# Optimization experiments

Measured on AMD Instinct MI355X. Metric: run time of the kernel, lower is better.

The kernel has to match this reference:

```python
import jax, jax.numpy as jnp
import numpy as np

N = 131072      # total nodes
G = 1024        # graphs
NPG = 128       # nodes per graph (equal-sized graphs, batch sorted)
E = 2097152     # edges (avg degree 16)
H = 64          # hidden_channels
K = 30          # sort-pool k
MAXZ = 1000     # max_z
D = 3 * H + 1   # total_latent_dim = hidden*num_layers + 1 = 193
DENSE = ((K - 2) // 2 + 1 - 5 + 1) * 32  # 352


def setup_inputs():
    key = jax.random.key(0)
    ks = jax.random.split(key, 16)
    z = jax.random.randint(ks[0], (N,), 0, MAXZ)
    # within-graph random edges
    g = jax.random.randint(ks[1], (E,), 0, G)
    src = g * NPG + jax.random.randint(ks[2], (E,), 0, NPG)
    dst = g * NPG + jax.random.randint(ks[3], (E,), 0, NPG)
    edge_index = jnp.stack([src, dst])
    batch = jnp.repeat(jnp.arange(G), NPG)

    def w(k, shape, fan):
        return jax.random.normal(k, shape, dtype=jnp.float32) / np.float32(np.sqrt(fan))

    z_table = w(ks[4], (MAXZ, H), H)
    W0 = w(ks[5], (H, H), H); b0 = jnp.zeros((H,), jnp.float32)
    W1 = w(ks[6], (H, H), H); b1 = jnp.zeros((H,), jnp.float32)
    W2 = w(ks[7], (H, H), H); b2 = jnp.zeros((H,), jnp.float32)
    W3 = w(ks[8], (H, 1), H); b3 = jnp.zeros((1,), jnp.float32)
    conv1_w = w(ks[9], (16, D), D); conv1_b = jnp.zeros((16,), jnp.float32)
    conv2_w = w(ks[10], (32, 16, 5), 16 * 5); conv2_b = jnp.zeros((32,), jnp.float32)
    lin1_w = w(ks[11], (DENSE, 128), DENSE); lin1_b = jnp.zeros((128,), jnp.float32)
    lin2_w = w(ks[12], (128, 1), 128); lin2_b = jnp.zeros((1,), jnp.float32)
    return dict(z=z, edge_index=edge_index, batch=batch, z_table=z_table,
                W0=W0, b0=b0, W1=W1, b1=b1, W2=W2, b2=b2, W3=W3, b3=b3,
                conv1_w=conv1_w, conv1_b=conv1_b, conv2_w=conv2_w, conv2_b=conv2_b,
                lin1_w=lin1_w, lin1_b=lin1_b, lin2_w=lin2_w, lin2_b=lin2_b)


def _forward(z, edge_index, z_table, W0, b0, W1, b1, W2, b2, W3, b3,
             conv1_w, conv1_b, conv2_w, conv2_b, lin1_w, lin1_b, lin2_w, lin2_b):
    src, dst = edge_index[0], edge_index[1]
    loop = jnp.arange(N)
    src_sl = jnp.concatenate([src, loop])  # self-loops (gcn_norm)
    dst_sl = jnp.concatenate([dst, loop])
    deg = jax.ops.segment_sum(jnp.ones((E + N,), jnp.float32), dst_sl, num_segments=N)
    dinv = jnp.where(deg > 0, 1.0 / jnp.sqrt(deg), 0.0)
    norm = dinv[src_sl] * dinv[dst_sl]  # sym-normalized edge weights

    def gcn(x, W, b):
        h = x @ W
        agg = jax.ops.segment_sum(h[src_sl] * norm[:, None], dst_sl, num_segments=N)
        return agg + b

    x = z_table[z]  # z_embedding lookup, [N, H]
    xs = []
    for W, b in ((W0, b0), (W1, b1), (W2, b2), (W3, b3)):
        x = jnp.tanh(gcn(x, W, b))
        xs.append(x)
    xc = jnp.concatenate(xs, axis=-1)  # [N, D] (concat of xs[1:])

    # global_sort_pool: sort per graph by last channel (descending), keep top-K.
    xg = xc.reshape(G, NPG, D)
    order = jnp.argsort(-xg[:, :, -1], axis=1)[:, :K]
    topk = jnp.take_along_axis(xg, order[:, :, None], axis=1)  # [G, K, D]

    # conv1: kernel=stride=D over flattened [G, 1, K*D] == per-node linear D->16
    h1 = jax.nn.relu(jnp.einsum('gkd,cd->gck', topk, conv1_w) + conv1_b[None, :, None])  # [G,16,K]
    p = h1.reshape(G, 16, K // 2, 2).max(-1)  # maxpool1d(2,2) -> [G,16,15]
    h2 = jax.nn.relu(
        jax.lax.conv_general_dilated(p, conv2_w, (1,), 'VALID',
                                     dimension_numbers=('NCH', 'OIH', 'NCH'))
        + conv2_b[None, :, None])  # [G,32,11]
    flat = h2.reshape(G, -1)  # channel-major flatten, matches torch .view
    hm = jax.nn.relu(flat @ lin1_w + lin1_b)  # MLP (dropout off in eval)
    return hm @ lin2_w + lin2_b  # [G, 1]


def reference(z, edge_index, batch, z_table, W0, b0, W1, b1, W2, b2, W3, b3,
              conv1_w, conv1_b, conv2_w, conv2_b, lin1_w, lin1_b, lin2_w, lin2_b):
    del batch  # graphs are equal-sized & node ids contiguous: reshape implements sort-pool segmentation
    return _forward(z, edge_index, z_table, W0, b0, W1, b1, W2, b2, W3, b3,
                    conv1_w, conv1_b, conv2_w, conv2_b, lin1_w, lin1_b, lin2_w, lin2_b)
```

## Files before the change

### kernel.cpp

```cpp
#include <hip/hip_runtime.h>

#define NGRAPH  1024
#define E_EDGES 2097152
#define ECAP    2944
#define MAXZ    1000

__device__ __forceinline__ float bfu_lo(unsigned u) { return __uint_as_float(u << 16); }
__device__ __forceinline__ float bfu_hi(unsigned u) { return __uint_as_float(u & 0xFFFF0000u); }
__device__ __forceinline__ unsigned packlo(float f0, float f1) {
    return (__float_as_uint(f0) >> 16) | (__float_as_uint(f1) & 0xFFFF0000u);
}
__device__ __forceinline__ int xh_idx(int r, int k)  { return (r << 6) | (k  ^ ((r & 7) << 3)); }
__device__ __forceinline__ int xl_idx(int r, int k2) { return (r << 5) | (k2 ^ ((r & 7) << 2)); }

__device__ __forceinline__ double tanh_fast(double p) {
    double q = 2.0 * p;
    q = fmin(40.0, fmax(-40.0, q));
    double nf = rint(q * 1.4426950408889634074);
    double r  = fma(nf, -6.93147180369123816490e-01, q);
    r = fma(nf, -1.90821492927058770002e-10, r);
    double er =     2.755731922398589e-07;
    er = fma(er, r, 2.755731922398589e-06);
    er = fma(er, r, 2.4801587301587302e-05);
    er = fma(er, r, 1.984126984126984e-04);
    er = fma(er, r, 1.3888888888888889e-03);
    er = fma(er, r, 8.333333333333333e-03);
    er = fma(er, r, 4.1666666666666664e-02);
    er = fma(er, r, 1.6666666666666666e-01);
    er = fma(er, r, 0.5);
    er = fma(er, r, 1.0);
    er = fma(er, r, 1.0);
    double E = er * __longlong_as_double((long long)(1023 + (int)nf) << 52);
    return 1.0 - 2.0 / (E + 1.0);
}

__global__ void markWS_kernel(float* out) {
    int i = blockIdx.x * 256 + threadIdx.x;
    if (i < NGRAPH) out[i] = 2.0f;
}

__global__ void adjscatter_kernel(const int* __restrict__ ei,
                                  unsigned* __restrict__ adjG) {
    int e = blockIdx.x * 256 + threadIdx.x;
    if (e >= E_EDGES) return;
    int s = ei[e];
    int d = ei[E_EDGES + e];
    int g = s >> 7;
    int sl = s & 127, dl = d & 127;
    atomicAdd(&adjG[((size_t)g << 12) + (dl << 5) + (sl >> 2)], 1u << ((sl & 3) << 3));
}

__global__ __launch_bounds__(1024, 1) void gnn2_kernel(
    const int* __restrict__ z,
    const unsigned* __restrict__ adjG,
    const float* __restrict__ zt,
    const float* __restrict__ W0, const float* __restrict__ b0,
    const float* __restrict__ W1, const float* __restrict__ b1,
    const float* __restrict__ W2, const float* __restrict__ b2,
    const float* __restrict__ W3, const float* __restrict__ b3,
    const float* __restrict__ c1w, const float* __restrict__ c1b,
    const float* __restrict__ c2w, const float* __restrict__ c2b,
    const float* __restrict__ l1w, const float* __restrict__ l1b,
    const float* __restrict__ l2w, const float* __restrict__ l2b,
    float* __restrict__ xdump,
    float* __restrict__ out)
{
    __shared__ __align__(16) float    Xhi[2][8192];
    __shared__ __align__(16) unsigned Xlo[2][4096];
    __shared__ unsigned char  csr[2][ECAP];
    __shared__ unsigned short rp16[2][132];
    __shared__ int            aux[2][128];
    __shared__ int            inv[2][30];
    __shared__ float          kd30f[2][30];
    __shared__ int            w0tot[2];

    const int half = threadIdx.x >> 9;
    const int tt   = threadIdx.x & 511;
    const int g    = (blockIdx.x << 1) | half;
    const int r0 = tt >> 3;
    const int r1 = r0 + 64;
    const int c0 = (tt & 7) << 3;

    float*          XH = Xhi[half];
    unsigned*       XL = Xlo[half];
    unsigned char*  CS = csr[half];
    unsigned short* RP = rp16[half];
    int*            AX = aux[half];

    unsigned* adjM = (unsigned*)XH;

    {
        const uint4* src = (const uint4*)(adjG + ((size_t)g << 12));
        uint4* dst = (uint4*)adjM;
        for (int i = tt; i < 1024; i += 512) dst[i] = src[i];
    }
    if (tt < 30) { inv[half][tt] = tt; kd30f[half][tt] = 0.f; }
    __syncthreads();

    int degv = 0;
    if (tt < 128) {
        for (int w = 0; w < 32; ++w) {
            unsigned u = adjM[(tt << 5) + w];
            degv += (int)((u & 255u) + ((u >> 8) & 255u) + ((u >> 16) & 255u) + (u >> 24));
        }
        AX[tt] = degv;
    }
    if (tt < 128) {
        int v = degv;
        for (int o = 1; o < 64; o <<= 1) {
            int u = __shfl_up(v, o, 64);
            if ((tt & 63) >= o) v += u;
        }
        if (tt == 63) w0tot[half] = v;
        RP[tt + 1] = (unsigned short)v;
    }
    __syncthreads();
    if (tt >= 64 && tt < 128) RP[tt + 1] = (unsigned short)(RP[tt + 1] + w0tot[half]);
    if (tt == 0) RP[0] = 0;
    __syncthreads();

    const int mydeg = (tt < 128) ? AX[tt] : 0;
    const double dv0 = 1.0 / sqrt((double)(AX[r0] + 1));
    const double dv1 = 1.0 / sqrt((double)(AX[r1] + 1));
    const double dvm = 1.0 / sqrt((double)(mydeg + 1));

    if (tt < 128) {
        unsigned pos = RP[tt];
        for (int w = 0; w < 32; ++w) {
            unsigned u = adjM[(tt << 5) + w];
            while (u) {
                int b2 = (u & 0xFFu) ? 0 : (u & 0xFF00u) ? 1 : (u & 0xFF0000u) ? 2 : 3;
                int m = (int)((u >> (b2 << 3)) & 255u);
                unsigned char sv = (unsigned char)((w << 2) + b2);
                for (int q = 0; q < m; ++q) { if (pos < ECAP) CS[pos] = sv; ++pos; }
                u &= ~(0xFFu << (b2 << 3));
            }
        }
    }
    __syncthreads();

    for (int idx = tt; idx < 8192; idx += 512) {
        int n = idx >> 6, c = idx & 63;
        int zv = z[(g << 7) + n];
        zv = (zv < 0) ? 0 : ((zv >= MAXZ) ? MAXZ - 1 : zv);
        XH[xh_idx(n, c)] = zt[zv * 64 + c];
    }
    __syncthreads();

    for (int layer = 0; layer < 3; ++layer) {
        const float* Wg = (layer == 0) ? W0 : (layer == 1) ? W1 : W2;
        const float* bg = (layer == 0) ? b0 : (layer == 1) ? b1 : b2;
        const bool haslo = (layer != 0);

        double accd0[8], accd1[8]; float accf0[8], accf1[8];
#pragma unroll
        for (int j = 0; j < 8; ++j) { accd0[j] = 0.0; accd1[j] = 0.0; accf0[j] = 0.f; accf1[j] = 0.f; }

        for (int k = 0; k < 64; k += 4) {
            float4 a0 = *(const float4*)&XH[xh_idx(r0, k)];
            float4 a1 = *(const float4*)&XH[xh_idx(r1, k)];
            float x0[4] = {a0.x, a0.y, a0.z, a0.w};
            float x1[4] = {a1.x, a1.y, a1.z, a1.w};
            float l0[4], l1[4];
            if (haslo) {
                uint2 u0 = *(const uint2*)&XL[xl_idx(r0, k >> 1)];
                uint2 u1 = *(const uint2*)&XL[xl_idx(r1, k >> 1)];
                l0[0] = bfu_lo(u0.x); l0[1] = bfu_hi(u0.x); l0[2] = bfu_lo(u0.y); l0[3] = bfu_hi(u0.y);
                l1[0] = bfu_lo(u1.x); l1[1] = bfu_hi(u1.x); l1[2] = bfu_lo(u1.y); l1[3] = bfu_hi(u1.y);
            }
#pragma unroll
            for (int kk = 0; kk < 4; ++kk) {
                const float* wr = Wg + ((k + kk) << 6) + c0;
                float4 wa = *(const float4*)wr;
                float4 wb = *(const float4*)(wr + 4);
                float wf[8] = {wa.x, wa.y, wa.z, wa.w, wb.x, wb.y, wb.z, wb.w};
                double xd0 = (double)x0[kk], xd1 = (double)x1[kk];
#pragma unroll
                for (int j = 0; j < 8; ++j) {
                    double wd = (double)wf[j];
                    accd0[j] = fma(xd0, wd, accd0[j]);
                    accd1[j] = fma(xd1, wd, accd1[j]);
                }
                if (haslo) {
#pragma unroll
                    for (int j = 0; j < 8; ++j) {
                        accf0[j] = fmaf(l0[kk], wf[j], accf0[j]);
                        accf1[j] = fmaf(l1[kk], wf[j], accf1[j]);
                    }
                }
            }
        }
        __syncthreads();

        float hfv[2][8], rsv[2][8];
#pragma unroll
        for (int rw = 0; rw < 2; ++rw) {
            int rr = rw ? r1 : r0;
            double dv = rw ? dv1 : dv0;
#pragma unroll
            for (int j = 0; j < 8; ++j) {
                double acc = rw ? (accd1[j] + (double)accf1[j]) : (accd0[j] + (double)accf0[j]);
                double h = dv * acc;
                float hf = (float)h;
                hfv[rw][j] = hf;
                rsv[rw][j] = (float)(h - (double)hf);
            }
            int bi = xh_idx(rr, c0);
            *(float4*)&XH[bi]     = make_float4(hfv[rw][0], hfv[rw][1], hfv[rw][2], hfv[rw][3]);
            *(float4*)&XH[bi + 4] = make_float4(hfv[rw][4], hfv[rw][5], hfv[rw][6], hfv[rw][7]);
            uint4 lv;
            lv.x = packlo(rsv[rw][0], rsv[rw][1]);
            lv.y = packlo(rsv[rw][2], rsv[rw][3]);
            lv.z = packlo(rsv[rw][4], rsv[rw][5]);
            lv.w = packlo(rsv[rw][6], rsv[rw][7]);
            *(uint4*)&XL[xl_idx(rr, c0 >> 1)] = lv;
        }
        __syncthreads();

        double ad[2][8]; float af[2][8];
#pragma unroll
        for (int rw = 0; rw < 2; ++rw)
#pragma unroll
            for (int j = 0; j < 8; ++j) { ad[rw][j] = (double)hfv[rw][j]; af[rw][j] = rsv[rw][j]; }

#pragma unroll
        for (int rw = 0; rw < 2; ++rw) {
            int rr = rw ? r1 : r0;
            for (unsigned e = RP[rr]; e < RP[rr + 1]; ++e) {
                int s = CS[e];
                int bi = (s << 6) | (c0 ^ ((s & 7) << 3));
                float4 a = *(const float4*)&XH[bi];
                float4 b = *(const float4*)&XH[bi + 4];
                uint4 lu = *(const uint4*)&XL[(s << 5) | ((c0 >> 1) ^ ((s & 7) << 2))];
                ad[rw][0] += (double)a.x; ad[rw][1] += (double)a.y;
                ad[rw][2] += (double)a.z; ad[rw][3] += (double)a.w;
                ad[rw][4] += (double)b.x; ad[rw][5] += (double)b.y;
                ad[rw][6] += (double)b.z; ad[rw][7] += (double)b.w;
                af[rw][0] += bfu_lo(lu.x); af[rw][1] += bfu_hi(lu.x);
                af[rw][2] += bfu_lo(lu.y); af[rw][3] += bfu_hi(lu.y);
                af[rw][4] += bfu_lo(lu.z); af[rw][5] += bfu_hi(lu.z);
                af[rw][6] += bfu_lo(lu.w); af[rw][7] += bfu_hi(lu.w);
            }
        }
        __syncthreads();

#pragma unroll
        for (int rw = 0; rw < 2; ++rw) {
            int rr = rw ? r1 : r0;
            double dv = rw ? dv1 : dv0;
            float vf[8], rs[8];
#pragma unroll
            for (int j = 0; j < 8; ++j) {
                double v = tanh_fast(dv * (ad[rw][j] + (double)af[rw][j]) + (double)bg[c0 + j]);
                float vfl = (float)v;
                vf[j] = vfl;
                rs[j] = (float)(v - (double)vfl);
            }
            int bi = xh_idx(rr, c0);
            *(float4*)&XH[bi]     = make_float4(vf[0], vf[1], vf[2], vf[3]);
            *(float4*)&XH[bi + 4] = make_float4(vf[4], vf[5], vf[6], vf[7]);
            uint4 lv;
            lv.x = packlo(rs[0], rs[1]);
            lv.y = packlo(rs[2], rs[3]);
            lv.z = packlo(rs[4], rs[5]);
            lv.w = packlo(rs[6], rs[7]);
            *(uint4*)&XL[xl_idx(rr, c0 >> 1)] = lv;

            if (layer < 2) {
                float* xd = xdump + (((size_t)g * 2 + layer) << 13) + (rr << 6) + c0;
                *(float4*)xd       = make_float4(vf[0], vf[1], vf[2], vf[3]);
                *(float4*)(xd + 4) = make_float4(vf[4], vf[5], vf[6], vf[7]);
            }
        }
        __syncthreads();
    }

    double* h4sD  = (double*)XL;
    double* keydD = ((double*)XL) + 128;

    double sdreg = 0.0;
    if (tt < 128) {
        double sd = 0.0; float sf = 0.f;
        for (int k = 0; k < 64; k += 4) {
            float4 a = *(const float4*)&XH[xh_idx(tt, k)];
            uint2  u = *(const uint2*)&XL[xl_idx(tt, k >> 1)];
            float4 w = *(const float4*)&W3[k];
            sd = fma((double)a.x, (double)w.x, sd);
            sd = fma((double)a.y, (double)w.y, sd);
            sd = fma((double)a.z, (double)w.z, sd);
            sd = fma((double)a.w, (double)w.w, sd);
            sf = fmaf(bfu_lo(u.x), w.x, sf);
            sf = fmaf(bfu_hi(u.x), w.y, sf);
            sf = fmaf(bfu_lo(u.y), w.z, sf);
            sf = fmaf(bfu_hi(u.y), w.w, sf);
        }
        sdreg = sd + (double)sf;
    }
    __syncthreads();
    if (tt < 128) h4sD[tt] = dvm * sdreg;
    __syncthreads();
    double keyreg = 0.0;
    if (tt < 128) {
        double a = h4sD[tt];
        for (unsigned e = RP[tt]; e < RP[tt + 1]; ++e) a += h4sD[CS[e]];
        keyreg = tanh_fast(dvm * a + (double)b3[0]);
        keydD[tt] = keyreg;
    }
    __syncthreads();

    if (tt < 128) {
        int rk = 0;
        for (int j = 0; j < 128; ++j) {
            double kj = keydD[j];
            if (kj > keyreg || (kj == keyreg && j < tt)) ++rk;
        }
        if (rk < 30) { inv[half][rk] = tt; kd30f[half][rk] = (float)keyreg; }
    }
    __syncthreads();

    float* XloF = (float*)XL;
    float* h1v = XloF + 2560;
    float* ppv = XloF + 3040;
    float* flv = XloF + 3280;
    float* hmv = XloF + 3632;

    if (tt < 480) {
        int c = tt & 15, k = tt >> 4;
        int node = inv[half][k];
        const float* wrow = c1w + c * 193;
        const float* xg0 = xdump + ((size_t)g * 2) * 8192 + node * 64;
        const float* xg1 = xg0 + 8192;
        float s8[8];
#pragma unroll
        for (int cg = 0; cg < 8; ++cg) {
            float acc = 0.f;
            float4 xa = *(const float4*)&xg0[cg * 8];
            float4 xb = *(const float4*)&xg0[cg * 8 + 4];
            const float* w0p = wrow + cg * 8;
            acc = fmaf(xa.x, w0p[0], acc); acc = fmaf(xa.y, w0p[1], acc);
            acc = fmaf(xa.z, w0p[2], acc); acc = fmaf(xa.w, w0p[3], acc);
            acc = fmaf(xb.x, w0p[4], acc); acc = fmaf(xb.y, w0p[5], acc);
            acc = fmaf(xb.z, w0p[6], acc); acc = fmaf(xb.w, w0p[7], acc);
            float4 ya = *(const float4*)&xg1[cg * 8];
            float4 yb = *(const float4*)&xg1[cg * 8 + 4];
            const float* w1p = wrow + 64 + cg * 8;
            acc = fmaf(ya.x, w1p[0], acc); acc = fmaf(ya.y, w1p[1], acc);
            acc = fmaf(ya.z, w1p[2], acc); acc = fmaf(ya.w, w1p[3], acc);
            acc = fmaf(yb.x, w1p[4], acc); acc = fmaf(yb.y, w1p[5], acc);
            acc = fmaf(yb.z, w1p[6], acc); acc = fmaf(yb.w, w1p[7], acc);
            const float* w2p = wrow + 128 + cg * 8;
#pragma unroll
            for (int j = 0; j < 8; ++j)
                acc = fmaf(XH[xh_idx(node, cg * 8 + j)], w2p[j], acc);
            s8[cg] = acc;
        }
        float A0 = s8[0] + s8[1], A1 = s8[2] + s8[3];
        float A2 = s8[4] + s8[5], A3 = s8[6] + s8[7];
        float G = (A0 + A1) + (A2 + A3);
        float s = G + c1w[c * 193 + 192] * kd30f[half][k] + c1b[c];
        h1v[c * 30 + k] = s > 0.f ? s : 0.f;
    }
    __syncthreads();
    if (tt < 240) {
        int c = tt & 15, i = tt >> 4;
        float a = h1v[c * 30 + 2 * i], b = h1v[c * 30 + 2 * i + 1];
        ppv[c * 15 + i] = a > b ? a : b;
    }
    __syncthreads();
    if (tt < 352) {
        int o = tt / 11, j = tt % 11;
        float s = c2b[o];
        for (int i = 0; i < 16; ++i)
#pragma unroll
            for (int u = 0; u < 5; ++u)
                s = fmaf(ppv[i * 15 + j + u], c2w[o * 80 + i * 5 + u], s);
        flv[tt] = s > 0.f ? s : 0.f;
    }
    __syncthreads();
    if (tt < 128) {
        float s = l1b[tt];
        for (int i = 0; i < 352; ++i) s = fmaf(flv[i], l1w[i * 128 + tt], s);
        hmv[tt] = s > 0.f ? s : 0.f;
    }
    __syncthreads();
    if (tt < 64) {
        float v = fmaf(hmv[tt], l2w[tt], hmv[tt + 64] * l2w[tt + 64]);
#pragma unroll
        for (int o = 32; o > 0; o >>= 1) v += __shfl_down(v, o, 64);
        if (tt == 0) out[g] = v + l2b[0];
    }
}

__global__ __launch_bounds__(512, 2) void gnn_kernel(
    const int* __restrict__ z,
    const unsigned* __restrict__ adjG,
    const float* __restrict__ zt,
    const float* __restrict__ W0, const float* __restrict__ b0,
    const float* __restrict__ W1, const float* __restrict__ b1,
    const float* __restrict__ W2, const float* __restrict__ b2,
    const float* __restrict__ W3, const float* __restrict__ b3,
    const float* __restrict__ c1w, const float* __restrict__ c1b,
    const float* __restrict__ c2w, const float* __restrict__ c2b,
    const float* __restrict__ l1w, const float* __restrict__ l1b,
    const float* __restrict__ l2w, const float* __restrict__ l2b,
    float* __restrict__ out)
{
    __shared__ __align__(16) float    Xhi[8192];
    __shared__ __align__(16) unsigned Xlo[4096];
    __shared__ unsigned char  csr[ECAP];
    __shared__ unsigned short rp16[132];
    __shared__ int            aux[128];
    __shared__ int            inv[30];
    __shared__ float          kd30f[30];
    __shared__ int            w0tot;

    const int g  = blockIdx.x;
    const int t  = threadIdx.x;
    const int r0 = t >> 3;
    const int r1 = r0 + 64;
    const int c0 = (t & 7) << 3;

    unsigned* adjM = (unsigned*)Xhi;

    {
        const uint4* src = (const uint4*)(adjG + ((size_t)g << 12));
        uint4* dst = (uint4*)adjM;
        for (int i = t; i < 1024; i += 512) dst[i] = src[i];
    }
    if (t < 30) { inv[t] = t; kd30f[t] = 0.f; }
    __syncthreads();

    int degv = 0;
    if (t < 128) {
        for (int w = 0; w < 32; ++w) {
            unsigned u = adjM[(t << 5) + w];
            degv += (int)((u & 255u) + ((u >> 8) & 255u) + ((u >> 16) & 255u) + (u >> 24));
        }
        aux[t] = degv;
    }
    if (t < 128) {
        int v = degv;
        for (int o = 1; o < 64; o <<= 1) {
            int u = __shfl_up(v, o, 64);
            if ((t & 63) >= o) v += u;
        }
        if (t == 63) w0tot = v;
        rp16[t + 1] = (unsigned short)v;
    }
    __syncthreads();
    if (t >= 64 && t < 128) rp16[t + 1] = (unsigned short)(rp16[t + 1] + w0tot);
    if (t == 0) rp16[0] = 0;
    __syncthreads();

    const int mydeg = (t < 128) ? aux[t] : 0;
    const double dv0 = 1.0 / sqrt((double)(aux[r0] + 1));
    const double dv1 = 1.0 / sqrt((double)(aux[r1] + 1));
    const double dvm = 1.0 / sqrt((double)(mydeg + 1));

    if (t < 128) {
        unsigned pos = rp16[t];
        for (int w = 0; w < 32; ++w) {
            unsigned u = adjM[(t << 5) + w];
            while (u) {
                int b2 = (u & 0xFFu) ? 0 : (u & 0xFF00u) ? 1 : (u & 0xFF0000u) ? 2 : 3;
                int m = (int)((u >> (b2 << 3)) & 255u);
                unsigned char sv = (unsigned char)((w << 2) + b2);
                for (int q = 0; q < m; ++q) { if (pos < ECAP) csr[pos] = sv; ++pos; }
                u &= ~(0xFFu << (b2 << 3));
            }
        }
    }
    __syncthreads();

    for (int idx = t; idx < 8192; idx += 512) {
        int n = idx >> 6, c = idx & 63;
        int zv = z[(g << 7) + n];
        zv = (zv < 0) ? 0 : ((zv >= MAXZ) ? MAXZ - 1 : zv);
        Xhi[xh_idx(n, c)] = zt[zv * 64 + c];
    }
    __syncthreads();

    float g1p[2][16];
#pragma unroll
    for (int rw = 0; rw < 2; ++rw)
#pragma unroll
        for (int c = 0; c < 16; ++c) g1p[rw][c] = 0.f;

    for (int layer = 0; layer < 3; ++layer) {
        const float* Wg = (layer == 0) ? W0 : (layer == 1) ? W1 : W2;
        const float* bg = (layer == 0) ? b0 : (layer == 1) ? b1 : b2;
        const bool haslo = (layer != 0);

        double accd0[8], accd1[8]; float accf0[8], accf1[8];
#pragma unroll
        for (int j = 0; j < 8; ++j) { accd0[j] = 0.0; accd1[j] = 0.0; accf0[j] = 0.f; accf1[j] = 0.f; }

        for (int k = 0; k < 64; k += 4) {
            float4 a0 = *(const float4*)&Xhi[xh_idx(r0, k)];
            float4 a1 = *(const float4*)&Xhi[xh_idx(r1, k)];
            float x0[4] = {a0.x, a0.y, a0.z, a0.w};
            float x1[4] = {a1.x, a1.y, a1.z, a1.w};
            float l0[4], l1[4];
            if (haslo) {
                uint2 u0 = *(const uint2*)&Xlo[xl_idx(r0, k >> 1)];
                uint2 u1 = *(const uint2*)&Xlo[xl_idx(r1, k >> 1)];
                l0[0] = bfu_lo(u0.x); l0[1] = bfu_hi(u0.x); l0[2] = bfu_lo(u0.y); l0[3] = bfu_hi(u0.y);
                l1[0] = bfu_lo(u1.x); l1[1] = bfu_hi(u1.x); l1[2] = bfu_lo(u1.y); l1[3] = bfu_hi(u1.y);
            }
#pragma unroll
            for (int kk = 0; kk < 4; ++kk) {
                const float* wr = Wg + ((k + kk) << 6) + c0;
                float4 wa = *(const float4*)wr;
                float4 wb = *(const float4*)(wr + 4);
                float wf[8] = {wa.x, wa.y, wa.z, wa.w, wb.x, wb.y, wb.z, wb.w};
                double xd0 = (double)x0[kk], xd1 = (double)x1[kk];
#pragma unroll
                for (int j = 0; j < 8; ++j) {
                    double wd = (double)wf[j];
                    accd0[j] = fma(xd0, wd, accd0[j]);
                    accd1[j] = fma(xd1, wd, accd1[j]);
                }
                if (haslo) {
#pragma unroll
                    for (int j = 0; j < 8; ++j) {
                        accf0[j] = fmaf(l0[kk], wf[j], accf0[j]);
                        accf1[j] = fmaf(l1[kk], wf[j], accf1[j]);
                    }
                }
            }
        }
        __syncthreads();

        float hfv[2][8], rsv[2][8];
#pragma unroll
        for (int rw = 0; rw < 2; ++rw) {
            int rr = rw ? r1 : r0;
            double dv = rw ? dv1 : dv0;
#pragma unroll
            for (int j = 0; j < 8; ++j) {
                double acc = rw ? (accd1[j] + (double)accf1[j]) : (accd0[j] + (double)accf0[j]);
                double h = dv * acc;
                float hf = (float)h;
                hfv[rw][j] = hf;
                rsv[rw][j] = (float)(h - (double)hf);
            }
            int bi = xh_idx(rr, c0);
            *(float4*)&Xhi[bi]     = make_float4(hfv[rw][0], hfv[rw][1], hfv[rw][2], hfv[rw][3]);
            *(float4*)&Xhi[bi + 4] = make_float4(hfv[rw][4], hfv[rw][5], hfv[rw][6], hfv[rw][7]);
            uint4 lv;
            lv.x = packlo(rsv[rw][0], rsv[rw][1]);
            lv.y = packlo(rsv[rw][2], rsv[rw][3]);
            lv.z = packlo(rsv[rw][4], rsv[rw][5]);
            lv.w = packlo(rsv[rw][6], rsv[rw][7]);
            *(uint4*)&Xlo[xl_idx(rr, c0 >> 1)] = lv;
        }
        __syncthreads();

        double ad[2][8]; float af[2][8];
#pragma unroll
        for (int rw = 0; rw < 2; ++rw)
#pragma unroll
            for (int j = 0; j < 8; ++j) { ad[rw][j] = (double)hfv[rw][j]; af[rw][j] = rsv[rw][j]; }

#pragma unroll
        for (int rw = 0; rw < 2; ++rw) {
            int rr = rw ? r1 : r0;
            for (unsigned e = rp16[rr]; e < rp16[rr + 1]; ++e) {
                int s = csr[e];
                int bi = (s << 6) | (c0 ^ ((s & 7) << 3));
                float4 a = *(const float4*)&Xhi[bi];
                float4 b = *(const float4*)&Xhi[bi + 4];
                uint4 lu = *(const uint4*)&Xlo[(s << 5) | ((c0 >> 1) ^ ((s & 7) << 2))];
                ad[rw][0] += (double)a.x; ad[rw][1] += (double)a.y;
                ad[rw][2] += (double)a.z; ad[rw][3] += (double)a.w;
                ad[rw][4] += (double)b.x; ad[rw][5] += (double)b.y;
                ad[rw][6] += (double)b.z; ad[rw][7] += (double)b.w;
                af[rw][0] += bfu_lo(lu.x); af[rw][1] += bfu_hi(lu.x);
                af[rw][2] += bfu_lo(lu.y); af[rw][3] += bfu_hi(lu.y);
                af[rw][4] += bfu_lo(lu.z); af[rw][5] += bfu_hi(lu.z);
                af[rw][6] += bfu_lo(lu.w); af[rw][7] += bfu_hi(lu.w);
            }
        }
        __syncthreads();

#pragma unroll
        for (int rw = 0; rw < 2; ++rw) {
            int rr = rw ? r1 : r0;
            double dv = rw ? dv1 : dv0;
            float vf[8], rs[8];
#pragma unroll
            for (int j = 0; j < 8; ++j) {
                double v = tanh_fast(dv * (ad[rw][j] + (double)af[rw][j]) + (double)bg[c0 + j]);
                float vfl = (float)v;
                vf[j] = vfl;
                rs[j] = (float)(v - (double)vfl);
            }
            int bi = xh_idx(rr, c0);
            *(float4*)&Xhi[bi]     = make_float4(vf[0], vf[1], vf[2], vf[3]);
            *(float4*)&Xhi[bi + 4] = make_float4(vf[4], vf[5], vf[6], vf[7]);
            uint4 lv;
            lv.x = packlo(rs[0], rs[1]);
            lv.y = packlo(rs[2], rs[3]);
            lv.z = packlo(rs[4], rs[5]);
            lv.w = packlo(rs[6], rs[7]);
            *(uint4*)&Xlo[xl_idx(rr, c0 >> 1)] = lv;

            const float* w1base = c1w + layer * 64 + c0;
            for (int c = 0; c < 16; ++c) {
                const float* wr = w1base + c * 193;
#pragma unroll
                for (int j = 0; j < 8; ++j)
                    g1p[rw][c] = fmaf(vf[j], wr[j], g1p[rw][c]);
            }
        }
        __syncthreads();
    }

    double* h4sD  = (double*)Xlo;
    double* keydD = ((double*)Xlo) + 128;

    double sdreg = 0.0;
    if (t < 128) {
        double sd = 0.0; float sf = 0.f;
        for (int k = 0; k < 64; k += 4) {
            float4 a = *(const float4*)&Xhi[xh_idx(t, k)];
            uint2  u = *(const uint2*)&Xlo[xl_idx(t, k >> 1)];
            float4 w = *(const float4*)&W3[k];
            sd = fma((double)a.x, (double)w.x, sd);
            sd = fma((double)a.y, (double)w.y, sd);
            sd = fma((double)a.z, (double)w.z, sd);
            sd = fma((double)a.w, (double)w.w, sd);
            sf = fmaf(bfu_lo(u.x), w.x, sf);
            sf = fmaf(bfu_hi(u.x), w.y, sf);
            sf = fmaf(bfu_lo(u.y), w.z, sf);
            sf = fmaf(bfu_hi(u.y), w.w, sf);
        }
        sdreg = sd + (double)sf;
    }
    __syncthreads();
    if (t < 128) h4sD[t] = dvm * sdreg;
    __syncthreads();
    double keyreg = 0.0;
    if (t < 128) {
        double a = h4sD[t];
        for (unsigned e = rp16[t]; e < rp16[t + 1]; ++e) a += h4sD[csr[e]];
        keyreg = tanh_fast(dvm * a + (double)b3[0]);
        keydD[t] = keyreg;
    }
    __syncthreads();

    if (t < 128) {
        int rk = 0;
        for (int j = 0; j < 128; ++j) {
            double kj = keydD[j];
            if (kj > keyreg || (kj == keyreg && j < t)) ++rk;
        }
        if (rk < 30) { inv[rk] = t; kd30f[rk] = (float)keyreg; }
    }

#pragma unroll
    for (int m = 1; m <= 4; m <<= 1) {
#pragma unroll
        for (int rw = 0; rw < 2; ++rw)
#pragma unroll
            for (int c = 0; c < 16; ++c)
                g1p[rw][c] += __shfl_xor(g1p[rw][c], m, 64);
    }
    __syncthreads();
    float* XloF = (float*)Xlo;
    float* G1   = XloF + 512;
    if ((t & 7) == 0) {
#pragma unroll
        for (int c = 0; c < 16; c += 4) {
            *(float4*)&G1[r0 * 16 + c] = make_float4(g1p[0][c], g1p[0][c + 1], g1p[0][c + 2], g1p[0][c + 3]);
            *(float4*)&G1[r1 * 16 + c] = make_float4(g1p[1][c], g1p[1][c + 1], g1p[1][c + 2], g1p[1][c + 3]);
        }
    }
    __syncthreads();

    float* h1v = XloF + 2560;
    float* ppv = XloF + 3040;
    float* flv = XloF + 3280;
    float* hmv = XloF + 3632;

    if (t < 480) {
        int c = t & 15, k = t >> 4;
        int node = inv[k];
        float s = G1[node * 16 + c] + c1w[c * 193 + 192] * kd30f[k] + c1b[c];
        h1v[c * 30 + k] = s > 0.f ? s : 0.f;
    }
    __syncthreads();
    if (t < 240) {
        int c = t & 15, i = t >> 4;
        float a = h1v[c * 30 + 2 * i], b = h1v[c * 30 + 2 * i + 1];
        ppv[c * 15 + i] = a > b ? a : b;
    }
    __syncthreads();
    if (t < 352) {
        int o = t / 11, j = t % 11;
        float s = c2b[o];
        for (int i = 0; i < 16; ++i)
#pragma unroll
            for (int u = 0; u < 5; ++u)
                s = fmaf(ppv[i * 15 + j + u], c2w[o * 80 + i * 5 + u], s);
        flv[t] = s > 0.f ? s : 0.f;
    }
    __syncthreads();
    if (t < 128) {
        float s = l1b[t];
        for (int i = 0; i < 352; ++i) s = fmaf(flv[i], l1w[i * 128 + t], s);
        hmv[t] = s > 0.f ? s : 0.f;
    }
    __syncthreads();
    if (t < 64) {
        float v = fmaf(hmv[t], l2w[t], hmv[t + 64] * l2w[t + 64]);
#pragma unroll
        for (int o = 32; o > 0; o >>= 1) v += __shfl_down(v, o, 64);
        if (t == 0) out[g] = v + l2b[0];
    }
}


extern "C" void kernel_launch(void* const* d_in, const int* in_sizes, int n_in,
                              void* d_out, int out_size, void* d_ws, size_t ws_size,
                              hipStream_t stream) {
    const int*   z   = (const int*)d_in[0];
    const int*   ei  = (const int*)d_in[1];
    const float* zt  = (const float*)d_in[3];
    const float* W0  = (const float*)d_in[4];
    const float* b0  = (const float*)d_in[5];
    const float* W1  = (const float*)d_in[6];
    const float* b1  = (const float*)d_in[7];
    const float* W2  = (const float*)d_in[8];
    const float* b2  = (const float*)d_in[9];
    const float* W3  = (const float*)d_in[10];
    const float* b3  = (const float*)d_in[11];
    const float* c1w = (const float*)d_in[12];
    const float* c1b = (const float*)d_in[13];
    const float* c2w = (const float*)d_in[14];
    const float* c2b = (const float*)d_in[15];
    const float* l1w = (const float*)d_in[16];
    const float* l1b = (const float*)d_in[17];
    const float* l2w = (const float*)d_in[18];
    const float* l2b = (const float*)d_in[19];
    float* out = (float*)d_out;

    const size_t ADJ_B = (size_t)NGRAPH * 4096 * 4;
    const size_t XD_B  = (size_t)NGRAPH * 2 * 8192 * 4;
    if (ws_size < ADJ_B) {
        markWS_kernel<<<4, 256, 0, stream>>>(out);
        return;
    }

    unsigned* adjG = (unsigned*)d_ws;

    hipMemsetAsync(adjG, 0, ADJ_B, stream);
    adjscatter_kernel<<<(E_EDGES + 255) / 256, 256, 0, stream>>>(ei, adjG);

    if (ws_size >= ADJ_B + XD_B) {
        float* xdump = (float*)((char*)d_ws + ADJ_B);
        gnn2_kernel<<<NGRAPH / 2, 1024, 0, stream>>>(z, adjG, zt,
                                                     W0, b0, W1, b1, W2, b2, W3, b3,
                                                     c1w, c1b, c2w, c2b, l1w, l1b, l2w, l2b,
                                                     xdump, out);
    } else {
        gnn_kernel<<<NGRAPH, 512, 0, stream>>>(z, adjG, zt,
                                               W0, b0, W1, b1, W2, b2, W3, b3,
                                               c1w, c1b, c2w, c2b, l1w, l1b, l2w, l2b,
                                               out);
    }
}
```

Baseline: 599.7 us.

## Process one graph per 1024-thread block with one node row per thread

The main kernel previously packed two graphs into each 1024-thread block, so each thread handled two node rows. It now launches one block per graph with 1024 threads, and each thread owns a single row. This halves the per-thread register state (double accumulators) and the serial edge-gather length, and it doubles the grid size. The cost is that shared memory per block is halved, so occupancy depends on whether two blocks can co-reside under launch_bounds(1024,1), and the serial tail phases now leave more threads idle per graph.

```diff
diff --git a/kernel.cpp b/kernel.cpp
--- a/kernel.cpp
+++ b/kernel.cpp
@@ -50,7 +50,7 @@
     atomicAdd(&adjG[((size_t)g << 12) + (dl << 5) + (sl >> 2)], 1u << ((sl & 3) << 3));
 }
 
-__global__ __launch_bounds__(1024, 1) void gnn2_kernel(
+__global__ __launch_bounds__(1024, 1) void gnn1k_kernel(
     const int* __restrict__ z,
     const unsigned* __restrict__ adjG,
     const float* __restrict__ zt,
@@ -65,85 +65,75 @@
     float* __restrict__ xdump,
     float* __restrict__ out)
 {
-    __shared__ __align__(16) float    Xhi[2][8192];
-    __shared__ __align__(16) unsigned Xlo[2][4096];
-    __shared__ unsigned char  csr[2][ECAP];
-    __shared__ unsigned short rp16[2][132];
-    __shared__ int            aux[2][128];
-    __shared__ int            inv[2][30];
-    __shared__ float          kd30f[2][30];
-    __shared__ int            w0tot[2];
-
-    const int half = threadIdx.x >> 9;
-    const int tt   = threadIdx.x & 511;
-    const int g    = (blockIdx.x << 1) | half;
-    const int r0 = tt >> 3;
-    const int r1 = r0 + 64;
-    const int c0 = (tt & 7) << 3;
-
-    float*          XH = Xhi[half];
-    unsigned*       XL = Xlo[half];
-    unsigned char*  CS = csr[half];
-    unsigned short* RP = rp16[half];
-    int*            AX = aux[half];
-
-    unsigned* adjM = (unsigned*)XH;
+    __shared__ __align__(16) float    Xhi[8192];
+    __shared__ __align__(16) unsigned Xlo[4096];
+    __shared__ unsigned char  csr[ECAP];
+    __shared__ unsigned short rp16[132];
+    __shared__ int            aux[128];
+    __shared__ int            inv[30];
+    __shared__ float          kd30f[30];
+    __shared__ int            w0tot;
+
+    const int g  = blockIdx.x;
+    const int t  = threadIdx.x;
+    const int r  = t >> 3;
+    const int c0 = (t & 7) << 3;
+
+    unsigned* adjM = (unsigned*)Xhi;
 
     {
         const uint4* src = (const uint4*)(adjG + ((size_t)g << 12));
-        uint4* dst = (uint4*)adjM;
-        for (int i = tt; i < 1024; i += 512) dst[i] = src[i];
-    }
-    if (tt < 30) { inv[half][tt] = tt; kd30f[half][tt] = 0.f; }
+        ((uint4*)adjM)[t & 1023] = src[t & 1023];
+    }
+    if (t < 30) { inv[t] = t; kd30f[t] = 0.f; }
     __syncthreads();
 
     int degv = 0;
-    if (tt < 128) {
+    if (t < 128) {
         for (int w = 0; w < 32; ++w) {
-            unsigned u = adjM[(tt << 5) + w];
+            unsigned u = adjM[(t << 5) + w];
             degv += (int)((u & 255u) + ((u >> 8) & 255u) + ((u >> 16) & 255u) + (u >> 24));
         }
-        AX[tt] = degv;
-    }
-    if (tt < 128) {
+        aux[t] = degv;
+    }
+    if (t < 128) {
         int v = degv;
         for (int o = 1; o < 64; o <<= 1) {
             int u = __shfl_up(v, o, 64);
-            if ((tt & 63) >= o) v += u;
-        }
-        if (tt == 63) w0tot[half] = v;
-        RP[tt + 1] = (unsigned short)v;
-    }
-    __syncthreads();
-    if (tt >= 64 && tt < 128) RP[tt + 1] = (unsigned short)(RP[tt + 1] + w0tot[half]);
-    if (tt == 0) RP[0] = 0;
-    __syncthreads();
-
-    const int mydeg = (tt < 128) ? AX[tt] : 0;
-    const double dv0 = 1.0 / sqrt((double)(AX[r0] + 1));
-    const double dv1 = 1.0 / sqrt((double)(AX[r1] + 1));
+            if ((t & 63) >= o) v += u;
+        }
+        if (t == 63) w0tot = v;
+        rp16[t + 1] = (unsigned short)v;
+    }
+    __syncthreads();
+    if (t >= 64 && t < 128) rp16[t + 1] = (unsigned short)(rp16[t + 1] + w0tot);
+    if (t == 0) rp16[0] = 0;
+    __syncthreads();
+
+    const int mydeg = (t < 128) ? aux[t] : 0;
+    const double dvr = 1.0 / sqrt((double)(aux[r] + 1));
     const double dvm = 1.0 / sqrt((double)(mydeg + 1));
 
-    if (tt < 128) {
-        unsigned pos = RP[tt];
+    if (t < 128) {
+        unsigned pos = rp16[t];
         for (int w = 0; w < 32; ++w) {
-            unsigned u = adjM[(tt << 5) + w];
+            unsigned u = adjM[(t << 5) + w];
             while (u) {
                 int b2 = (u & 0xFFu) ? 0 : (u & 0xFF00u) ? 1 : (u & 0xFF0000u) ? 2 : 3;
                 int m = (int)((u >> (b2 << 3)) & 255u);
                 unsigned char sv = (unsigned char)((w << 2) + b2);
-                for (int q = 0; q < m; ++q) { if (pos < ECAP) CS[pos] = sv; ++pos; }
+                for (int q = 0; q < m; ++q) { if (pos < ECAP) csr[pos] = sv; ++pos; }
                 u &= ~(0xFFu << (b2 << 3));
             }
         }
     }
     __syncthreads();
 
-    for (int idx = tt; idx < 8192; idx += 512) {
+    for (int idx = t; idx < 8192; idx += 1024) {
         int n = idx >> 6, c = idx & 63;
         int zv = z[(g << 7) + n];
         zv = (zv < 0) ? 0 : ((zv >= MAXZ) ? MAXZ - 1 : zv);
-        XH[xh_idx(n, c)] = zt[zv * 64 + c];
+        Xhi[xh_idx(n, c)] = zt[zv * 64 + c];
     }
     __syncthreads();
 
@@ -152,21 +142,17 @@
         const float* bg = (layer == 0) ? b0 : (layer == 1) ? b1 : b2;
         const bool haslo = (layer != 0);
 
-        double accd0[8], accd1[8]; float accf0[8], accf1[8];
-#pragma unroll
-        for (int j = 0; j < 8; ++j) { accd0[j] = 0.0; accd1[j] = 0.0; accf0[j] = 0.f; accf1[j] = 0.f; }
+        double accd[8]; float accf[8];
+#pragma unroll
+        for (int j = 0; j < 8; ++j) { accd[j] = 0.0; accf[j] = 0.f; }
 
         for (int k = 0; k < 64; k += 4) {
-            float4 a0 = *(const float4*)&XH[xh_idx(r0, k)];
-            float4 a1 = *(const float4*)&XH[xh_idx(r1, k)];
+            float4 a0 = *(const float4*)&Xhi[xh_idx(r, k)];
             float x0[4] = {a0.x, a0.y, a0.z, a0.w};
-            float x1[4] = {a1.x, a1.y, a1.z, a1.w};
-            float l0[4], l1[4];
+            float l0[4];
             if (haslo) {
-                uint2 u0 = *(const uint2*)&XL[xl_idx(r0, k >> 1)];
-                uint2 u1 = *(const uint2*)&XL[xl_idx(r1, k >> 1)];
+                uint2 u0 = *(const uint2*)&Xlo[xl_idx(r, k >> 1)];
                 l0[0] = bfu_lo(u0.x); l0[1] = bfu_hi(u0.x); l0[2] = bfu_lo(u0.y); l0[3] = bfu_hi(u0.y);
-                l1[0] = bfu_lo(u1.x); l1[1] = bfu_hi(u1.x); l1[2] = bfu_lo(u1.y); l1[3] = bfu_hi(u1.y);
             }
 #pragma unroll
             for (int kk = 0; kk < 4; ++kk) {
@@ -174,100 +160,82 @@
                 float4 wa = *(const float4*)wr;
                 float4 wb = *(const float4*)(wr + 4);
                 float wf[8] = {wa.x, wa.y, wa.z, wa.w, wb.x, wb.y, wb.z, wb.w};
-                double xd0 = (double)x0[kk], xd1 = (double)x1[kk];
-#pragma unroll
-                for (int j = 0; j < 8; ++j) {
-                    double wd = (double)wf[j];
-                    accd0[j] = fma(xd0, wd, accd0[j]);
-                    accd1[j] = fma(xd1, wd, accd1[j]);
+                double xd0 = (double)x0[kk];
+#pragma unroll
+                for (int j = 0; j < 8; ++j)
+                    accd[j] = fma(xd0, (double)wf[j], accd[j]);
+                if (haslo) {
+#pragma unroll
+                    for (int j = 0; j < 8; ++j)
+                        accf[j] = fmaf(l0[kk], wf[j], accf[j]);
                 }
-                if (haslo) {
-#pragma unroll
-                    for (int j = 0; j < 8; ++j) {
-                        accf0[j] = fmaf(l0[kk], wf[j], accf0[j]);
-                        accf1[j] = fmaf(l1[kk], wf[j], accf1[j]);
-                    }
-                }
             }
         }
         __syncthreads();
 
-        float hfv[2][8], rsv[2][8];
-#pragma unroll
-        for (int rw = 0; rw < 2; ++rw) {
-            int rr = rw ? r1 : r0;
-            double dv = rw ? dv1 : dv0;
-#pragma unroll
-            for (int j = 0; j < 8; ++j) {
-                double acc = rw ? (accd1[j] + (double)accf1[j]) : (accd0[j] + (double)accf0[j]);
-                double h = dv * acc;
-                float hf = (float)h;
-                hfv[rw][j] = hf;
-                rsv[rw][j] = (float)(h - (double)hf);
-            }
-            int bi = xh_idx(rr, c0);
-            *(float4*)&XH[bi]     = make_float4(hfv[rw][0], hfv[rw][1], hfv[rw][2], hfv[rw][3]);
-            *(float4*)&XH[bi + 4] = make_float4(hfv[rw][4], hfv[rw][5], hfv[rw][6], hfv[rw][7]);
-            uint4 lv;
-            lv.x = packlo(rsv[rw][0], rsv[rw][1]);
-            lv.y = packlo(rsv[rw][2], rsv[rw][3]);
-            lv.z = packlo(rsv[rw][4], rsv[rw][5]);
-            lv.w = packlo(rsv[rw][6], rsv[rw][7]);
-            *(uint4*)&XL[xl_idx(rr, c0 >> 1)] = lv;
-        }
-        __syncthreads();
-
-        double ad[2][8]; float af[2][8];
-#pragma unroll
-        for (int rw = 0; rw < 2; ++rw)
-#pragma unroll
-            for (int j = 0; j < 8; ++j) { ad[rw][j] = (double)hfv[rw][j]; af[rw][j] = rsv[rw][j]; }
-
-#pragma unroll
-        for (int rw = 0; rw < 2; ++rw) {
-            int rr = rw ? r1 : r0;
-            for (unsigned e = RP[rr]; e < RP[rr + 1]; ++e) {
-                int s = CS[e];
-                int bi = (s << 6) | (c0 ^ ((s & 7) << 3));
-                float4 a = *(const float4*)&XH[bi];
-                float4 b = *(const float4*)&XH[bi + 4];
-                uint4 lu = *(const uint4*)&XL[(s << 5) | ((c0 >> 1) ^ ((s & 7) << 2))];
-                ad[rw][0] += (double)a.x; ad[rw][1] += (double)a.y;
-                ad[rw][2] += (double)a.z; ad[rw][3] += (double)a.w;
-                ad[rw][4] += (double)b.x; ad[rw][5] += (double)b.y;
-                ad[rw][6] += (double)b.z; ad[rw][7] += (double)b.w;
-                af[rw][0] += bfu_lo(lu.x); af[rw][1] += bfu_hi(lu.x);
-                af[rw][2] += bfu_lo(lu.y); af[rw][3] += bfu_hi(lu.y);
-                af[rw][4] += bfu_lo(lu.z); af[rw][5] += bfu_hi(lu.z);
-                af[rw][6] += bfu_lo(lu.w); af[rw][7] += bfu_hi(lu.w);
-            }
-        }
-        __syncthreads();
-
-#pragma unroll
-        for (int rw = 0; rw < 2; ++rw) {
-            int rr = rw ? r1 : r0;
-            double dv = rw ? dv1 : dv0;
-            float vf[8], rs[8];
-#pragma unroll
-            for (int j = 0; j < 8; ++j) {
-                double v = tanh_fast(dv * (ad[rw][j] + (double)af[rw][j]) + (double)bg[c0 + j]);
-                float vfl = (float)v;
-                vf[j] = vfl;
-                rs[j] = (float)(v - (double)vfl);
-            }
-            int bi = xh_idx(rr, c0);
-            *(float4*)&XH[bi]     = make_float4(vf[0], vf[1], vf[2], vf[3]);
-            *(float4*)&XH[bi + 4] = make_float4(vf[4], vf[5], vf[6], vf[7]);
+        float hf[8], rs[8];
+#pragma unroll
+        for (int j = 0; j < 8; ++j) {
+            double h = dvr * (accd[j] + (double)accf[j]);
+            float hfl = (float)h;
+            hf[j] = hfl;
+            rs[j] = (float)(h - (double)hfl);
+        }
+        {
+            int bi = xh_idx(r, c0);
+            *(float4*)&Xhi[bi]     = make_float4(hf[0], hf[1], hf[2], hf[3]);
+            *(float4*)&Xhi[bi + 4] = make_float4(hf[4], hf[5], hf[6], hf[7]);
             uint4 lv;
             lv.x = packlo(rs[0], rs[1]);
             lv.y = packlo(rs[2], rs[3]);
             lv.z = packlo(rs[4], rs[5]);
             lv.w = packlo(rs[6], rs[7]);
-            *(uint4*)&XL[xl_idx(rr, c0 >> 1)] = lv;
+            *(uint4*)&Xlo[xl_idx(r, c0 >> 1)] = lv;
+        }
+        __syncthreads();
+
+        double ad[8]; float af[8];
+#pragma unroll
+        for (int j = 0; j < 8; ++j) { ad[j] = (double)hf[j]; af[j] = rs[j]; }
+
+        for (unsigned e = rp16[r]; e < rp16[r + 1]; ++e) {
+            int s = csr[e];
+            int bi = (s << 6) | (c0 ^ ((s & 7) << 3));
+            float4 a = *(const float4*)&Xhi[bi];
+            float4 b = *(const float4*)&Xhi[bi + 4];
+            uint4 lu = *(const uint4*)&Xlo[(s << 5) | ((c0 >> 1) ^ ((s & 7) << 2))];
+            ad[0] += (double)a.x; ad[1] += (double)a.y;
+            ad[2] += (double)a.z; ad[3] += (double)a.w;
+            ad[4] += (double)b.x; ad[5] += (double)b.y;
+            ad[6] += (double)b.z; ad[7] += (double)b.w;
+            af[0] += bfu_lo(lu.x); af[1] += bfu_hi(lu.x);
+            af[2] += bfu_lo(lu.y); af[3] += bfu_hi(lu.y);
+            af[4] += bfu_lo(lu.z); af[5] += bfu_hi(lu.z);
+            af[6] += bfu_lo(lu.w); af[7] += bfu_hi(lu.w);
+        }
+        __syncthreads();
+
+        {
+            float vf[8], rs2[8];
+#pragma unroll
+            for (int j = 0; j < 8; ++j) {
+                double v = tanh_fast(dvr * (ad[j] + (double)af[j]) + (double)bg[c0 + j]);
+                float vfl = (float)v;
+                vf[j] = vfl;
+                rs2[j] = (float)(v - (double)vfl);
+            }
+            int bi = xh_idx(r, c0);
+            *(float4*)&Xhi[bi]     = make_float4(vf[0], vf[1], vf[2], vf[3]);
+            *(float4*)&Xhi[bi + 4] = make_float4(vf[4], vf[5], vf[6], vf[7]);
+            uint4 lv;
+            lv.x = packlo(rs2[0], rs2[1]);
+            lv.y = packlo(rs2[2], rs2[3]);
+            lv.z = packlo(rs2[4], rs2[5]);
+            lv.w = packlo(rs2[6], rs2[7]);
+            *(uint4*)&Xlo[xl_idx(r, c0 >> 1)] = lv;
 
             if (layer < 2) {
-                float* xd = xdump + (((size_t)g * 2 + layer) << 13) + (rr << 6) + c0;
+                float* xd = xdump + (((size_t)g * 2 + layer) << 13) + (r << 6) + c0;
                 *(float4*)xd       = make_float4(vf[0], vf[1], vf[2], vf[3]);
                 *(float4*)(xd + 4) = make_float4(vf[4], vf[5], vf[6], vf[7]);
             }
@@ -275,15 +243,15 @@
         __syncthreads();
     }
 
-    double* h4sD  = (double*)XL;
-    double* keydD = ((double*)XL) + 128;
+    double* h4sD  = (double*)Xlo;
+    double* keydD = ((double*)Xlo) + 128;
 
     double sdreg = 0.0;
-    if (tt < 128) {
+    if (t < 128) {
         double sd = 0.0; float sf = 0.f;
         for (int k = 0; k < 64; k += 4) {
-            float4 a = *(const float4*)&XH[xh_idx(tt, k)];
-            uint2  u = *(const uint2*)&XL[xl_idx(tt, k >> 1)];
+            float4 a = *(const float4*)&Xhi[xh_idx(t, k)];
+            uint2  u = *(const uint2*)&Xlo[xl_idx(t, k >> 1)];
             float4 w = *(const float4*)&W3[k];
             sd = fma((double)a.x, (double)w.x, sd);
             sd = fma((double)a.y, (double)w.y, sd);
@@ -297,36 +265,36 @@
         sdreg = sd + (double)sf;
     }
     __syncthreads();
-    if (tt < 128) h4sD[tt] = dvm * sdreg;
+    if (t < 128) h4sD[t] = dvm * sdreg;
     __syncthreads();
     double keyreg = 0.0;
-    if (tt < 128) {
-        double a = h4sD[tt];
-        for (unsigned e = RP[tt]; e < RP[tt + 1]; ++e) a += h4sD[CS[e]];
+    if (t < 128) {
+        double a = h4sD[t];
+        for (unsigned e = rp16[t]; e < rp16[t + 1]; ++e) a += h4sD[csr[e]];
         keyreg = tanh_fast(dvm * a + (double)b3[0]);
-        keydD[tt] = keyreg;
-    }
-    __syncthreads();
-
-    if (tt < 128) {
+        keydD[t] = keyreg;
+    }
+    __syncthreads();
+
+    if (t < 128) {
         int rk = 0;
         for (int j = 0; j < 128; ++j) {
             double kj = keydD[j];
-            if (kj > keyreg || (kj == keyreg && j < tt)) ++rk;
-        }
-        if (rk < 30) { inv[half][rk] = tt; kd30f[half][rk] = (float)keyreg; }
-    }
-    __syncthreads();
-
-    float* XloF = (float*)XL;
+            if (kj > keyreg || (kj == keyreg && j < t)) ++rk;
+        }
+        if (rk < 30) { inv[rk] = t; kd30f[rk] = (float)keyreg; }
+    }
+    __syncthreads();
+
+    float* XloF = (float*)Xlo;
     float* h1v = XloF + 2560;
     float* ppv = XloF + 3040;
     float* flv = XloF + 3280;
     float* hmv = XloF + 3632;
 
-    if (tt < 480) {
-        int c = tt & 15, k = tt >> 4;
-        int node = inv[half][k];
+    if (t < 480) {
+        int c = t & 15, k = t >> 4;
+        int node = inv[k];
         const float* wrow = c1w + c * 193;
         const float* xg0 = xdump + ((size_t)g * 2) * 8192 + node * 64;
         const float* xg1 = xg0 + 8192;
@@ -351,43 +319,43 @@
             const float* w2p = wrow + 128 + cg * 8;
 #pragma unroll
             for (int j = 0; j < 8; ++j)
-                acc = fmaf(XH[xh_idx(node, cg * 8 + j)], w2p[j], acc);
+                acc = fmaf(Xhi[xh_idx(node, cg * 8 + j)], w2p[j], acc);
             s8[cg] = acc;
         }
         float A0 = s8[0] + s8[1], A1 = s8[2] + s8[3];
         float A2 = s8[4] + s8[5], A3 = s8[6] + s8[7];
         float G = (A0 + A1) + (A2 + A3);
-        float s = G + c1w[c * 193 + 192] * kd30f[half][k] + c1b[c];
+        float s = G + c1w[c * 193 + 192] * kd30f[k] + c1b[c];
         h1v[c * 30 + k] = s > 0.f ? s : 0.f;
     }
     __syncthreads();
-    if (tt < 240) {
-        int c = tt & 15, i = tt >> 4;
+    if (t < 240) {
+        int c = t & 15, i = t >> 4;
         float a = h1v[c * 30 + 2 * i], b = h1v[c * 30 + 2 * i + 1];
         ppv[c * 15 + i] = a > b ? a : b;
     }
     __syncthreads();
-    if (tt < 352) {
-        int o = tt / 11, j = tt % 11;
+    if (t < 352) {
+        int o = t / 11, j = t % 11;
         float s = c2b[o];
         for (int i = 0; i < 16; ++i)
 #pragma unroll
             for (int u = 0; u < 5; ++u)
                 s = fmaf(ppv[i * 15 + j + u], c2w[o * 80 + i * 5 + u], s);
-        flv[tt] = s > 0.f ? s : 0.f;
-    }
-    __syncthreads();
-    if (tt < 128) {
-        float s = l1b[tt];
-        for (int i = 0; i < 352; ++i) s = fmaf(flv[i], l1w[i * 128 + tt], s);
-        hmv[tt] = s > 0.f ? s : 0.f;
-    }
-    __syncthreads();
-    if (tt < 64) {
-        float v = fmaf(hmv[tt], l2w[tt], hmv[tt + 64] * l2w[tt + 64]);
+        flv[t] = s > 0.f ? s : 0.f;
+    }
+    __syncthreads();
+    if (t < 128) {
+        float s = l1b[t];
+        for (int i = 0; i < 352; ++i) s = fmaf(flv[i], l1w[i * 128 + t], s);
+        hmv[t] = s > 0.f ? s : 0.f;
+    }
+    __syncthreads();
+    if (t < 64) {
+        float v = fmaf(hmv[t], l2w[t], hmv[t + 64] * l2w[t + 64]);
 #pragma unroll
         for (int o = 32; o > 0; o >>= 1) v += __shfl_down(v, o, 64);
-        if (tt == 0) out[g] = v + l2b[0];
+        if (t == 0) out[g] = v + l2b[0];
     }
 }
 
@@ -759,10 +727,10 @@
 
     if (ws_size >= ADJ_B + XD_B) {
         float* xdump = (float*)((char*)d_ws + ADJ_B);
-        gnn2_kernel<<<NGRAPH / 2, 1024, 0, stream>>>(z, adjG, zt,
-                                                     W0, b0, W1, b1, W2, b2, W3, b3,
-                                                     c1w, c1b, c2w, c2b, l1w, l1b, l2w, l2b,
-                                                     xdump, out);
+        gnn1k_kernel<<<NGRAPH, 1024, 0, stream>>>(z, adjG, zt,
+                                                  W0, b0, W1, b1, W2, b2, W3, b3,
+                                                  c1w, c1b, c2w, c2b, l1w, l1b, l2w, l2b,
+                                                  xdump, out);
     } else {
         gnn_kernel<<<NGRAPH, 512, 0, stream>>>(z, adjG, zt,
                                                W0, b0, W1, b1, W2, b2, W3, b3,
```

New measurement: 741.8 us. 23.7% more time.
